# Kernel tuning notes

Hardware: AMD Instinct MI355X
Metric: run time of the kernel (lower is better)

The kernel has to match this reference:

```python
import jax, jax.numpy as jnp
import numpy as np

B, C, L = 8192, 256, 80          # nodes(batch), channels = out_channels*4, seq_len
OUT, HID, FD = 64, 128, 128      # out_channels, hidden dims, feature_dim
WIN, STR = 10, 5                 # sliding window
NW = (L - WIN) // STR + 1        # 15 windows
NT = B * NW                      # temporal nodes = 122880
E_S, E_T = 262144, 983040


def _param_shapes(prefix):
    return [(prefix + "l1_W", (C, HID)), (prefix + "l1_b", (HID,)), (prefix + "l1_Wr", (C, HID)),
            (prefix + "l2_W", (HID, OUT)), (prefix + "l2_b", (OUT,)), (prefix + "l2_Wr", (HID, OUT)),
            (prefix + "p1_W", (OUT, FD)), (prefix + "p1_b", (FD,)), (prefix + "p2_W", (FD, FD)), (prefix + "p2_b", (FD,))]


def setup_inputs():
    key = jax.random.key(0)
    shapes = _param_shapes("s_") + _param_shapes("t_")
    ks = jax.random.split(key, len(shapes) + 3)
    inp = {"x": jax.random.normal(ks[0], (B, C, L), jnp.float32),
           "spatial_edge_index": jax.random.randint(ks[1], (2, E_S), 0, B),
           "temporal_edge_index": jax.random.randint(ks[2], (2, E_T), 0, NT)}
    for i, (name, sh) in enumerate(shapes):
        scale = 1.0 / np.sqrt(sh[0]) if len(sh) == 2 else 0.01
        inp[name] = scale * jax.random.normal(ks[3 + i], sh, jnp.float32)
    return inp


def _l2norm(x):
    return x / jnp.maximum(jnp.linalg.norm(x, axis=1, keepdims=True), 1e-12)


def _sage(x, src, dst, Wl, b, Wr, n):
    # PyG SAGEConv (mean aggr): lin_l(mean_{j->i} x_j) + lin_r(x_i)
    agg = jax.ops.segment_sum(x[src], dst, num_segments=n)
    cnt = jax.ops.segment_sum(jnp.ones((src.shape[0],), x.dtype), dst, num_segments=n)
    mean = agg / jnp.maximum(cnt, 1.0)[:, None]
    return mean @ Wl + b + x @ Wr


def _encoder(x, ei, p, n):
    src, dst = ei[0], ei[1]
    h = jax.nn.relu(_sage(x, src, dst, p[0], p[1], p[2], n))
    h = _sage(h, src, dst, p[3], p[4], p[5], n)
    return _l2norm(h)


def _proj(x, W1, b1, W2, b2):
    return _l2norm(jax.nn.relu(x @ W1 + b1) @ W2 + b2)


def _forward(x, sp, tp, spatial_edge_index, temporal_edge_index):
    feats = x  # feature_extractor = identity
    node_x = feats.mean(axis=-1)                     # [B, C]
    s_emb = _encoder(node_x, spatial_edge_index, sp[:6], B)
    s_proj = _proj(s_emb, *sp[6:])
    # sliding window mean reduction, vectorized
    starts = jnp.arange(0, L - WIN + 1, STR)
    idx = starts[:, None] + jnp.arange(WIN)
    red = feats[:, :, idx].mean(axis=-1)             # [B, C, NW]
    red = red.transpose(0, 2, 1).reshape(NT, C)      # [B*NW, C]
    t_emb = _encoder(red, temporal_edge_index, tp[:6], NT)
    t_emb = t_emb.reshape(B, NW, OUT).mean(axis=1)   # [B, OUT]
    t_proj = _proj(t_emb, *tp[6:])
    return s_proj, t_proj


def reference(x, spatial_edge_index, temporal_edge_index,
              s_l1_W, s_l1_b, s_l1_Wr, s_l2_W, s_l2_b, s_l2_Wr, s_p1_W, s_p1_b, s_p2_W, s_p2_b,
              t_l1_W, t_l1_b, t_l1_Wr, t_l2_W, t_l2_b, t_l2_Wr, t_p1_W, t_p1_b, t_p2_W, t_p2_b):
    sp = (s_l1_W, s_l1_b, s_l1_Wr, s_l2_W, s_l2_b, s_l2_Wr, s_p1_W, s_p1_b, s_p2_W, s_p2_b)
    tp = (t_l1_W, t_l1_b, t_l1_Wr, t_l2_W, t_l2_b, t_l2_Wr, t_p1_W, t_p1_b, t_p2_W, t_p2_b)
    return _forward(x, sp, tp, spatial_edge_index, temporal_edge_index)
```

## Files before the change

kernel.cpp:

```cpp
#include <hip/hip_runtime.h>

#define B_    8192
#define C_    256
#define L_    80
#define OUT_  64
#define HID_  128
#define FD_   128
#define NW_   15
#define NT_   122880
#define E_S_  262144
#define E_T_  983040

__global__ __launch_bounds__(256) void k_reduce_x(const float* __restrict__ x,
                                                  float* __restrict__ node_x,
                                                  float* __restrict__ red) {
    int gid = blockIdx.x * 256 + threadIdx.x;
    const float4* row4 = reinterpret_cast<const float4*>(x + (size_t)gid * L_);
    float v[L_];
#pragma unroll
    for (int i = 0; i < L_ / 4; ++i) {
        float4 t = row4[i];
        v[4*i+0] = t.x; v[4*i+1] = t.y; v[4*i+2] = t.z; v[4*i+3] = t.w;
    }
    float s5[16];
    float tot = 0.f;
#pragma unroll
    for (int j = 0; j < 16; ++j) {
        float s = 0.f;
#pragma unroll
        for (int k = 0; k < 5; ++k) s += v[5*j + k];
        s5[j] = s; tot += s;
    }
    node_x[gid] = tot * (1.f / L_);
    int b = gid >> 8;
    int c = gid & 255;
#pragma unroll
    for (int w = 0; w < NW_; ++w)
        red[((size_t)(b * NW_ + w)) * C_ + c] = (s5[w] + s5[w + 1]) * 0.1f;
}

#define BM 64
#define BN 64
#define BK 16
__global__ __launch_bounds__(256) void k_gemm(const float* __restrict__ A,
                                              const float* __restrict__ W,
                                              const float* __restrict__ bias,
                                              float* __restrict__ Co,
                                              int N, int K, int M, int relu) {
    __shared__ float As[BK][BM];
    __shared__ float Ws[BK][BN];
    int t = threadIdx.x;
    int row0 = blockIdx.x * BM;
    int col0 = blockIdx.y * BN;
    int lr = t >> 2;
    int lk = (t & 3) * 4;
    int wk = t >> 4;
    int wc = (t & 15) * 4;
    int ty = t >> 4;
    int tx = t & 15;
    float acc[4][4] = {};
    for (int k0 = 0; k0 < K; k0 += BK) {
        float4 av = *reinterpret_cast<const float4*>(&A[(size_t)(row0 + lr) * K + k0 + lk]);
        float4 wv = *reinterpret_cast<const float4*>(&W[(size_t)(k0 + wk) * M + col0 + wc]);
        __syncthreads();
        As[lk + 0][lr] = av.x; As[lk + 1][lr] = av.y;
        As[lk + 2][lr] = av.z; As[lk + 3][lr] = av.w;
        *reinterpret_cast<float4*>(&Ws[wk][wc]) = wv;
        __syncthreads();
#pragma unroll
        for (int kk = 0; kk < BK; ++kk) {
            float4 a  = *reinterpret_cast<const float4*>(&As[kk][ty * 4]);
            float4 w4 = *reinterpret_cast<const float4*>(&Ws[kk][tx * 4]);
            acc[0][0] += a.x * w4.x; acc[0][1] += a.x * w4.y; acc[0][2] += a.x * w4.z; acc[0][3] += a.x * w4.w;
            acc[1][0] += a.y * w4.x; acc[1][1] += a.y * w4.y; acc[1][2] += a.y * w4.z; acc[1][3] += a.y * w4.w;
            acc[2][0] += a.z * w4.x; acc[2][1] += a.z * w4.y; acc[2][2] += a.z * w4.z; acc[2][3] += a.z * w4.w;
            acc[3][0] += a.w * w4.x; acc[3][1] += a.w * w4.y; acc[3][2] += a.w * w4.z; acc[3][3] += a.w * w4.w;
        }
    }
    int cbase = col0 + tx * 4;
    float4 bv = make_float4(0.f, 0.f, 0.f, 0.f);
    if (bias) bv = *reinterpret_cast<const float4*>(&bias[cbase]);
#pragma unroll
    for (int i = 0; i < 4; ++i) {
        int r = row0 + ty * 4 + i;
        float4 o;
        o.x = acc[i][0] + bv.x; o.y = acc[i][1] + bv.y;
        o.z = acc[i][2] + bv.z; o.w = acc[i][3] + bv.w;
        if (relu) {
            o.x = fmaxf(o.x, 0.f); o.y = fmaxf(o.y, 0.f);
            o.z = fmaxf(o.z, 0.f); o.w = fmaxf(o.w, 0.f);
        }
        *reinterpret_cast<float4*>(&Co[(size_t)r * M + cbase]) = o;
    }
}

__global__ __launch_bounds__(256) void k_gemm_dual(const float* __restrict__ A,
                                                   const float* __restrict__ W1,
                                                   float* __restrict__ C1,
                                                   const float* __restrict__ W2,
                                                   const float* __restrict__ b2,
                                                   float* __restrict__ C2,
                                                   int N, int K, int M) {
    __shared__ float As[BK][BM];
    __shared__ float W1s[BK][BN];
    __shared__ float W2s[BK][BN];
    int t = threadIdx.x;
    int row0 = blockIdx.x * BM;
    int col0 = blockIdx.y * BN;
    int lr = t >> 2;
    int lk = (t & 3) * 4;
    int wk = t >> 4;
    int wc = (t & 15) * 4;
    int ty = t >> 4;
    int tx = t & 15;
    float acc1[4][4] = {};
    float acc2[4][4] = {};
    for (int k0 = 0; k0 < K; k0 += BK) {
        float4 av  = *reinterpret_cast<const float4*>(&A[(size_t)(row0 + lr) * K + k0 + lk]);
        float4 w1v = *reinterpret_cast<const float4*>(&W1[(size_t)(k0 + wk) * M + col0 + wc]);
        float4 w2v = *reinterpret_cast<const float4*>(&W2[(size_t)(k0 + wk) * M + col0 + wc]);
        __syncthreads();
        As[lk + 0][lr] = av.x; As[lk + 1][lr] = av.y;
        As[lk + 2][lr] = av.z; As[lk + 3][lr] = av.w;
        *reinterpret_cast<float4*>(&W1s[wk][wc]) = w1v;
        *reinterpret_cast<float4*>(&W2s[wk][wc]) = w2v;
        __syncthreads();
#pragma unroll
        for (int kk = 0; kk < BK; ++kk) {
            float4 a  = *reinterpret_cast<const float4*>(&As[kk][ty * 4]);
            float4 u  = *reinterpret_cast<const float4*>(&W1s[kk][tx * 4]);
            float4 w  = *reinterpret_cast<const float4*>(&W2s[kk][tx * 4]);
            acc1[0][0] += a.x * u.x; acc1[0][1] += a.x * u.y; acc1[0][2] += a.x * u.z; acc1[0][3] += a.x * u.w;
            acc1[1][0] += a.y * u.x; acc1[1][1] += a.y * u.y; acc1[1][2] += a.y * u.z; acc1[1][3] += a.y * u.w;
            acc1[2][0] += a.z * u.x; acc1[2][1] += a.z * u.y; acc1[2][2] += a.z * u.z; acc1[2][3] += a.z * u.w;
            acc1[3][0] += a.w * u.x; acc1[3][1] += a.w * u.y; acc1[3][2] += a.w * u.z; acc1[3][3] += a.w * u.w;
            acc2[0][0] += a.x * w.x; acc2[0][1] += a.x * w.y; acc2[0][2] += a.x * w.z; acc2[0][3] += a.x * w.w;
            acc2[1][0] += a.y * w.x; acc2[1][1] += a.y * w.y; acc2[1][2] += a.y * w.z; acc2[1][3] += a.y * w.w;
            acc2[2][0] += a.z * w.x; acc2[2][1] += a.z * w.y; acc2[2][2] += a.z * w.z; acc2[2][3] += a.z * w.w;
            acc2[3][0] += a.w * w.x; acc2[3][1] += a.w * w.y; acc2[3][2] += a.w * w.z; acc2[3][3] += a.w * w.w;
        }
    }
    int cbase = col0 + tx * 4;
    float4 bv = *reinterpret_cast<const float4*>(&b2[cbase]);
#pragma unroll
    for (int i = 0; i < 4; ++i) {
        int r = row0 + ty * 4 + i;
        float4 o1, o2;
        o1.x = acc1[i][0]; o1.y = acc1[i][1]; o1.z = acc1[i][2]; o1.w = acc1[i][3];
        o2.x = acc2[i][0] + bv.x; o2.y = acc2[i][1] + bv.y;
        o2.z = acc2[i][2] + bv.z; o2.w = acc2[i][3] + bv.w;
        *reinterpret_cast<float4*>(&C1[(size_t)r * M + cbase]) = o1;
        *reinterpret_cast<float4*>(&C2[(size_t)r * M + cbase]) = o2;
    }
}

__global__ __launch_bounds__(256) void k_cnt(const int* __restrict__ dst,
                                             int* __restrict__ cnt, int E) {
    int g = blockIdx.x * 256 + threadIdx.x;
    if (g < E) atomicAdd(&cnt[dst[g]], 1);
}

__global__ __launch_bounds__(256) void k_scan_blk(const int* __restrict__ cnt,
                                                  int* __restrict__ rs,
                                                  int* __restrict__ bsum, int N) {
    __shared__ int s[256];
    int g = blockIdx.x * 256 + threadIdx.x;
    int v = (g < N) ? cnt[g] : 0;
    s[threadIdx.x] = v;
    __syncthreads();
    for (int off = 1; off < 256; off <<= 1) {
        int t = (threadIdx.x >= off) ? s[threadIdx.x - off] : 0;
        __syncthreads();
        s[threadIdx.x] += t;
        __syncthreads();
    }
    if (g < N) rs[g] = s[threadIdx.x] - v;
    if (threadIdx.x == 255) bsum[blockIdx.x] = s[255];
}

__global__ void k_scan_top(int* __restrict__ bsum, int nb) {
    if (threadIdx.x == 0 && blockIdx.x == 0) {
        int acc = 0;
        for (int i = 0; i < nb; ++i) { int v = bsum[i]; bsum[i] = acc; acc += v; }
    }
}

__global__ __launch_bounds__(256) void k_scan_add(int* __restrict__ rs,
                                                  const int* __restrict__ bsum,
                                                  int* __restrict__ fill, int N) {
    int g = blockIdx.x * 256 + threadIdx.x;
    if (g < N) {
        int v = rs[g] + bsum[blockIdx.x];
        rs[g] = v;
        fill[g] = v;
    }
}

__global__ __launch_bounds__(256) void k_scatter(const int* __restrict__ src,
                                                 const int* __restrict__ dst,
                                                 int* __restrict__ fill,
                                                 int* __restrict__ csr, int E) {
    int g = blockIdx.x * 256 + threadIdx.x;
    if (g < E) {
        int p = atomicAdd(&fill[dst[g]], 1);
        csr[p] = src[g];
    }
}

__global__ __launch_bounds__(256) void k_agg128(const int* __restrict__ rs,
                                                const int* __restrict__ cnt,
                                                const int* __restrict__ csr,
                                                const float* __restrict__ Y,
                                                const float* __restrict__ Z,
                                                float* __restrict__ Hout, int N) {
    int wid = (blockIdx.x * 256 + threadIdx.x) >> 6;
    int lane = threadIdx.x & 63;
    if (wid >= N) return;
    int s0 = rs[wid], c = cnt[wid];
    float2 acc = make_float2(0.f, 0.f);
    int j = 0;
    for (; j + 1 < c; j += 2) {
        int sa = csr[s0 + j], sb = csr[s0 + j + 1];
        float2 va = *reinterpret_cast<const float2*>(&Y[(size_t)sa * 128 + lane * 2]);
        float2 vb = *reinterpret_cast<const float2*>(&Y[(size_t)sb * 128 + lane * 2]);
        acc.x += va.x + vb.x; acc.y += va.y + vb.y;
    }
    if (j < c) {
        int sa = csr[s0 + j];
        float2 va = *reinterpret_cast<const float2*>(&Y[(size_t)sa * 128 + lane * 2]);
        acc.x += va.x; acc.y += va.y;
    }
    float rc = 1.f / fmaxf((float)c, 1.f);
    size_t idx = (size_t)wid * 128 + lane * 2;
    float2 z = *reinterpret_cast<const float2*>(&Z[idx]);
    float2 o;
    o.x = fmaxf(acc.x * rc + z.x, 0.f);
    o.y = fmaxf(acc.y * rc + z.y, 0.f);
    *reinterpret_cast<float2*>(&Hout[idx]) = o;
}

__global__ __launch_bounds__(256) void k_agg64n(const int* __restrict__ rs,
                                                const int* __restrict__ cnt,
                                                const int* __restrict__ csr,
                                                const float* __restrict__ Y,
                                                const float* __restrict__ Z,
                                                float* __restrict__ emb, int N) {
    int wid = (blockIdx.x * 256 + threadIdx.x) >> 6;
    int lane = threadIdx.x & 63;
    if (wid >= N) return;
    int s0 = rs[wid], c = cnt[wid];
    float acc = 0.f;
    int j = 0;
    for (; j + 1 < c; j += 2) {
        int sa = csr[s0 + j], sb = csr[s0 + j + 1];
        acc += Y[(size_t)sa * 64 + lane] + Y[(size_t)sb * 64 + lane];
    }
    if (j < c) acc += Y[(size_t)csr[s0 + j] * 64 + lane];
    float rc = 1.f / fmaxf((float)c, 1.f);
    size_t idx = (size_t)wid * 64 + lane;
    float v = acc * rc + Z[idx];
    float ss = v * v;
#pragma unroll
    for (int m = 32; m; m >>= 1) ss += __shfl_xor(ss, m, 64);
    float inv = 1.f / fmaxf(sqrtf(ss), 1e-12f);
    emb[idx] = v * inv;
}

__global__ __launch_bounds__(256) void k_l2n128(const float* __restrict__ in,
                                                float* __restrict__ out, int N) {
    int wid = (blockIdx.x * 256 + threadIdx.x) >> 6;
    int lane = threadIdx.x & 63;
    if (wid >= N) return;
    size_t idx = (size_t)wid * 128 + lane * 2;
    float2 v = *reinterpret_cast<const float2*>(&in[idx]);
    float ss = v.x * v.x + v.y * v.y;
#pragma unroll
    for (int m = 32; m; m >>= 1) ss += __shfl_xor(ss, m, 64);
    float inv = 1.f / fmaxf(sqrtf(ss), 1e-12f);
    float2 o; o.x = v.x * inv; o.y = v.y * inv;
    *reinterpret_cast<float2*>(&out[idx]) = o;
}

__global__ __launch_bounds__(256) void k_tmean(const float* __restrict__ emb,
                                               float* __restrict__ out) {
    int gid = blockIdx.x * 256 + threadIdx.x;
    if (gid >= B_ * OUT_) return;
    int b = gid >> 6;
    int o = gid & 63;
    float s = 0.f;
#pragma unroll
    for (int w = 0; w < NW_; ++w) s += emb[((size_t)(b * NW_ + w)) * OUT_ + o];
    out[gid] = s * (1.f / NW_);
}

extern "C" void kernel_launch(void* const* d_in, const int* in_sizes, int n_in,
                              void* d_out, int out_size, void* d_ws, size_t ws_size,
                              hipStream_t stream) {
    const float* x      = (const float*)d_in[0];
    const int*   s_ei   = (const int*)d_in[1];
    const int*   t_ei   = (const int*)d_in[2];
    const float* s_l1_W  = (const float*)d_in[3];
    const float* s_l1_b  = (const float*)d_in[4];
    const float* s_l1_Wr = (const float*)d_in[5];
    const float* s_l2_W  = (const float*)d_in[6];
    const float* s_l2_b  = (const float*)d_in[7];
    const float* s_l2_Wr = (const float*)d_in[8];
    const float* s_p1_W  = (const float*)d_in[9];
    const float* s_p1_b  = (const float*)d_in[10];
    const float* s_p2_W  = (const float*)d_in[11];
    const float* s_p2_b  = (const float*)d_in[12];
    const float* t_l1_W  = (const float*)d_in[13];
    const float* t_l1_b  = (const float*)d_in[14];
    const float* t_l1_Wr = (const float*)d_in[15];
    const float* t_l2_W  = (const float*)d_in[16];
    const float* t_l2_b  = (const float*)d_in[17];
    const float* t_l2_Wr = (const float*)d_in[18];
    const float* t_p1_W  = (const float*)d_in[19];
    const float* t_p1_b  = (const float*)d_in[20];
    const float* t_p2_W  = (const float*)d_in[21];
    const float* t_p2_b  = (const float*)d_in[22];

    const int* s_src = s_ei, *s_dst = s_ei + E_S_;
    const int* t_src = t_ei, *t_dst = t_ei + E_T_;

    float* ws   = (float*)d_ws;
    float* dout = (float*)d_out;

    float* red    = ws + 0;
    float* nodex  = ws + 31457280;
    float* sY     = ws + 33554432;
    float* sZ     = ws + 34603008;
    float* sH     = ws + 35651584;
    float* s2Y    = ws + 36700160;
    float* s2Z    = ws + 37224448;
    float* sE     = ws + 37748736;
    float* sP     = ws + 38273024;
    float* sT     = ws + 39321600;
    float* tY     = ws + 31457280;
    float* tZ     = ws + 47185920;
    float* tH     = ws + 0;
    float* t2Y    = ws + 15728640;
    float* t2Z    = ws + 23592960;
    float* tE     = ws + 31457280;
    float* tM     = ws + 39321600;
    float* tP     = ws + 39845888;
    float* tT     = ws + 40894464;
    int* s_cnt  = (int*)(ws + 62914560);
    int* s_rs   = (int*)(ws + 62922752);
    int* s_fill = (int*)(ws + 62930944);
    int* s_csr  = (int*)(ws + 62939136);
    int* t_cnt  = (int*)(ws + 63201280);
    int* t_rs   = (int*)(ws + 63324160);
    int* t_fill = (int*)(ws + 63447040);
    int* t_csr  = (int*)(ws + 63569920);
    int* bsum   = (int*)(ws + 64552960);

    k_reduce_x<<<(B_ * C_) / 256, 256, 0, stream>>>(x, nodex, red);

    hipMemsetAsync(s_cnt, 0, (size_t)B_ * 4, stream);
    k_cnt<<<E_S_ / 256, 256, 0, stream>>>(s_dst, s_cnt, E_S_);
    k_scan_blk<<<B_ / 256, 256, 0, stream>>>(s_cnt, s_rs, bsum, B_);
    k_scan_top<<<1, 1, 0, stream>>>(bsum, B_ / 256);
    k_scan_add<<<B_ / 256, 256, 0, stream>>>(s_rs, bsum, s_fill, B_);
    k_scatter<<<E_S_ / 256, 256, 0, stream>>>(s_src, s_dst, s_fill, s_csr, E_S_);

    k_gemm_dual<<<dim3(B_ / 64, HID_ / 64), 256, 0, stream>>>(nodex, s_l1_W, sY, s_l1_Wr, s_l1_b, sZ, B_, C_, HID_);
    k_agg128<<<B_ / 4, 256, 0, stream>>>(s_rs, s_cnt, s_csr, sY, sZ, sH, B_);
    k_gemm_dual<<<dim3(B_ / 64, OUT_ / 64), 256, 0, stream>>>(sH, s_l2_W, s2Y, s_l2_Wr, s_l2_b, s2Z, B_, HID_, OUT_);
    k_agg64n<<<B_ / 4, 256, 0, stream>>>(s_rs, s_cnt, s_csr, s2Y, s2Z, sE, B_);
    k_gemm<<<dim3(B_ / 64, FD_ / 64), 256, 0, stream>>>(sE, s_p1_W, s_p1_b, sP, B_, OUT_, FD_, 1);
    k_gemm<<<dim3(B_ / 64, FD_ / 64), 256, 0, stream>>>(sP, s_p2_W, s_p2_b, sT, B_, FD_, FD_, 0);
    k_l2n128<<<B_ / 4, 256, 0, stream>>>(sT, dout, B_);

    hipMemsetAsync(t_cnt, 0, (size_t)NT_ * 4, stream);
    k_cnt<<<E_T_ / 256, 256, 0, stream>>>(t_dst, t_cnt, E_T_);
    k_scan_blk<<<NT_ / 256, 256, 0, stream>>>(t_cnt, t_rs, bsum, NT_);
    k_scan_top<<<1, 1, 0, stream>>>(bsum, NT_ / 256);
    k_scan_add<<<NT_ / 256, 256, 0, stream>>>(t_rs, bsum, t_fill, NT_);
    k_scatter<<<E_T_ / 256, 256, 0, stream>>>(t_src, t_dst, t_fill, t_csr, E_T_);

    k_gemm_dual<<<dim3(NT_ / 64, HID_ / 64), 256, 0, stream>>>(red, t_l1_W, tY, t_l1_Wr, t_l1_b, tZ, NT_, C_, HID_);
    k_agg128<<<NT_ / 4, 256, 0, stream>>>(t_rs, t_cnt, t_csr, tY, tZ, tH, NT_);
    k_gemm_dual<<<dim3(NT_ / 64, OUT_ / 64), 256, 0, stream>>>(tH, t_l2_W, t2Y, t_l2_Wr, t_l2_b, t2Z, NT_, HID_, OUT_);
    k_agg64n<<<NT_ / 4, 256, 0, stream>>>(t_rs, t_cnt, t_csr, t2Y, t2Z, tE, NT_);
    k_tmean<<<(B_ * OUT_) / 256, 256, 0, stream>>>(tE, tM);
    k_gemm<<<dim3(B_ / 64, FD_ / 64), 256, 0, stream>>>(tM, t_p1_W, t_p1_b, tP, B_, OUT_, FD_, 1);
    k_gemm<<<dim3(B_ / 64, FD_ / 64), 256, 0, stream>>>(tP, t_p2_W, t_p2_b, tT, B_, FD_, FD_, 0);
    k_l2n128<<<B_ / 4, 256, 0, stream>>>(tT, dout + (size_t)B_ * FD_, B_);
}
```

Measured before the change: 1.704 ms.

## Run SAGE linear layers on MFMA with split-bf16 hi/lo emulation of fp32

Replaces the fp32 SIMT dual GEMMs of both SAGE layers with bf16 MFMA kernels that use a hi/lo split (three MFMAs per tile) to approximate fp32 accuracy. Activations are written as bf16 hi/lo pairs by the reduction and aggregation kernels, and the weights are converted and transposed once per call by a new kernel. The single-thread top-level scan becomes a parallel 512-thread scan. The aim is to move the large temporal GEMMs onto matrix cores, at the cost of twice the activation traffic for the hi/lo planes, separate launches per weight matrix, and a small accuracy loss from dropping the lo*lo term.

```diff
diff --git a/kernel.cpp b/kernel.cpp
--- a/kernel.cpp
+++ b/kernel.cpp
@@ -11,9 +11,24 @@
 #define E_S_  262144
 #define E_T_  983040
 
+typedef unsigned short ushort_t;
+typedef __attribute__((ext_vector_type(8))) short bf16x8;
+typedef __attribute__((ext_vector_type(4))) float f32x4;
+
+__device__ inline void split_bf16(float a, ushort_t& h, ushort_t& l) {
+    unsigned u = __float_as_uint(a);
+    unsigned hb = (u + 0x7FFFu + ((u >> 16) & 1u)) & 0xFFFF0000u;
+    h = (ushort_t)(hb >> 16);
+    float r = a - __uint_as_float(hb);
+    unsigned v = __float_as_uint(r);
+    l = (ushort_t)((v + 0x7FFFu + ((v >> 16) & 1u)) >> 16);
+}
+
 __global__ __launch_bounds__(256) void k_reduce_x(const float* __restrict__ x,
-                                                  float* __restrict__ node_x,
-                                                  float* __restrict__ red) {
+                                                  ushort_t* __restrict__ node_h,
+                                                  ushort_t* __restrict__ node_l,
+                                                  ushort_t* __restrict__ red_h,
+                                                  ushort_t* __restrict__ red_l) {
     int gid = blockIdx.x * 256 + threadIdx.x;
     const float4* row4 = reinterpret_cast<const float4*>(x + (size_t)gid * L_);
     float v[L_];
@@ -31,12 +46,256 @@
         for (int k = 0; k < 5; ++k) s += v[5*j + k];
         s5[j] = s; tot += s;
     }
-    node_x[gid] = tot * (1.f / L_);
+    ushort_t h, l;
+    split_bf16(tot * (1.f / L_), h, l);
+    node_h[gid] = h; node_l[gid] = l;
     int b = gid >> 8;
     int c = gid & 255;
 #pragma unroll
-    for (int w = 0; w < NW_; ++w)
-        red[((size_t)(b * NW_ + w)) * C_ + c] = (s5[w] + s5[w + 1]) * 0.1f;
+    for (int w = 0; w < NW_; ++w) {
+        split_bf16((s5[w] + s5[w + 1]) * 0.1f, h, l);
+        size_t idx = ((size_t)(b * NW_ + w)) * C_ + c;
+        red_h[idx] = h; red_l[idx] = l;
+    }
+}
+
+__global__ __launch_bounds__(256) void k_conv_all(
+        const float* __restrict__ w0, const float* __restrict__ w1,
+        const float* __restrict__ w2, const float* __restrict__ w3,
+        const float* __restrict__ w4, const float* __restrict__ w5,
+        const float* __restrict__ w6, const float* __restrict__ w7,
+        ushort_t* __restrict__ blob) {
+    const int bstart[9] = {0, 128, 256, 288, 320, 448, 576, 608, 640};
+    const int Ks[8]     = {256, 256, 128, 128, 256, 256, 128, 128};
+    const int hoff[8]   = {0, 65536, 131072, 147456, 163840, 229376, 294912, 311296};
+    int blk = blockIdx.x;
+    int seg = 0;
+    while (blk >= bstart[seg + 1]) ++seg;
+    const float* W = (seg == 0) ? w0 : (seg == 1) ? w1 : (seg == 2) ? w2 : (seg == 3) ? w3
+                   : (seg == 4) ? w4 : (seg == 5) ? w5 : (seg == 6) ? w6 : w7;
+    int K = Ks[seg];
+    int nel = (bstart[seg + 1] - bstart[seg]) * 256;
+    int M = nel / K;
+    int g = (blk - bstart[seg]) * 256 + threadIdx.x;
+    int k = g / M, m = g - k * M;
+    ushort_t h, l;
+    split_bf16(W[g], h, l);
+    blob[hoff[seg] + m * K + k] = h;
+    blob[hoff[seg] + nel + m * K + k] = l;
+}
+
+template<int KTOT, int NF>
+__global__ __launch_bounds__(256, 2) void k_mfma_gemm(const ushort_t* __restrict__ Ah,
+                                                      const ushort_t* __restrict__ Al,
+                                                      const ushort_t* __restrict__ Wh,
+                                                      const ushort_t* __restrict__ Wl,
+                                                      const float* __restrict__ bias,
+                                                      float* __restrict__ C) {
+    constexpr int BN = NF * 32;
+    __shared__ short sAh[128][72], sAl[128][72], sWh[128][72], sWl[128][72];
+    int t = threadIdx.x;
+    int row0 = blockIdx.x * 128;
+    int wid = t >> 6, lane = t & 63;
+    int wr = wid >> 1, wc = wid & 1;
+    int lrow = lane & 15, lkg = lane >> 4;
+
+    f32x4 acc[4][NF];
+#pragma unroll
+    for (int mi = 0; mi < 4; ++mi)
+#pragma unroll
+        for (int ni = 0; ni < NF; ++ni) {
+            acc[mi][ni].x = 0.f; acc[mi][ni].y = 0.f;
+            acc[mi][ni].z = 0.f; acc[mi][ni].w = 0.f;
+        }
+
+    for (int k0 = 0; k0 < KTOT; k0 += 64) {
+        __syncthreads();
+#pragma unroll
+        for (int i = 0; i < 4; ++i) {
+            int ch = t + i * 256;
+            int r = ch >> 3, c = ch & 7;
+            *reinterpret_cast<int4*>(&sAh[r][c * 8]) =
+                *reinterpret_cast<const int4*>(&Ah[(size_t)(row0 + r) * KTOT + k0 + c * 8]);
+            *reinterpret_cast<int4*>(&sAl[r][c * 8]) =
+                *reinterpret_cast<const int4*>(&Al[(size_t)(row0 + r) * KTOT + k0 + c * 8]);
+        }
+#pragma unroll
+        for (int i = 0; i < 4; ++i) {
+            int ch = t + i * 256;
+            int r = ch >> 3, c = ch & 7;
+            if (r < BN) {
+                *reinterpret_cast<int4*>(&sWh[r][c * 8]) =
+                    *reinterpret_cast<const int4*>(&Wh[(size_t)r * KTOT + k0 + c * 8]);
+                *reinterpret_cast<int4*>(&sWl[r][c * 8]) =
+                    *reinterpret_cast<const int4*>(&Wl[(size_t)r * KTOT + k0 + c * 8]);
+            }
+        }
+        __syncthreads();
+#pragma unroll
+        for (int ks = 0; ks < 64; ks += 32) {
+            bf16x8 ah[4], al[4], wh[NF], wl[NF];
+            int kk = ks + lkg * 8;
+#pragma unroll
+            for (int mi = 0; mi < 4; ++mi) {
+                int r = wr * 64 + mi * 16 + lrow;
+                ah[mi] = *reinterpret_cast<const bf16x8*>(&sAh[r][kk]);
+                al[mi] = *reinterpret_cast<const bf16x8*>(&sAl[r][kk]);
+            }
+#pragma unroll
+            for (int ni = 0; ni < NF; ++ni) {
+                int r = wc * (NF * 16) + ni * 16 + lrow;
+                wh[ni] = *reinterpret_cast<const bf16x8*>(&sWh[r][kk]);
+                wl[ni] = *reinterpret_cast<const bf16x8*>(&sWl[r][kk]);
+            }
+#pragma unroll
+            for (int mi = 0; mi < 4; ++mi)
+#pragma unroll
+                for (int ni = 0; ni < NF; ++ni) {
+                    acc[mi][ni] = __builtin_amdgcn_mfma_f32_16x16x32_bf16(ah[mi], wh[ni], acc[mi][ni], 0, 0, 0);
+                    acc[mi][ni] = __builtin_amdgcn_mfma_f32_16x16x32_bf16(ah[mi], wl[ni], acc[mi][ni], 0, 0, 0);
+                    acc[mi][ni] = __builtin_amdgcn_mfma_f32_16x16x32_bf16(al[mi], wh[ni], acc[mi][ni], 0, 0, 0);
+                }
+        }
+    }
+    float bv[NF];
+#pragma unroll
+    for (int ni = 0; ni < NF; ++ni) {
+        int gcol = wc * (NF * 16) + ni * 16 + lrow;
+        bv[ni] = bias ? bias[gcol] : 0.f;
+    }
+#pragma unroll
+    for (int mi = 0; mi < 4; ++mi)
+#pragma unroll
+        for (int ni = 0; ni < NF; ++ni) {
+            int gcol = wc * (NF * 16) + ni * 16 + lrow;
+#pragma unroll
+            for (int j = 0; j < 4; ++j) {
+                int grow = row0 + wr * 64 + mi * 16 + lkg * 4 + j;
+                C[(size_t)grow * BN + gcol] = acc[mi][ni][j] + bv[ni];
+            }
+        }
+}
+
+__global__ __launch_bounds__(256) void k_cnt(const int* __restrict__ dst,
+                                             int* __restrict__ cnt, int E) {
+    int g = blockIdx.x * 256 + threadIdx.x;
+    if (g < E) atomicAdd(&cnt[dst[g]], 1);
+}
+
+__global__ __launch_bounds__(256) void k_scan_blk(const int* __restrict__ cnt,
+                                                  int* __restrict__ rs,
+                                                  int* __restrict__ bsum, int N) {
+    __shared__ int s[256];
+    int g = blockIdx.x * 256 + threadIdx.x;
+    int v = (g < N) ? cnt[g] : 0;
+    s[threadIdx.x] = v;
+    __syncthreads();
+    for (int off = 1; off < 256; off <<= 1) {
+        int t = (threadIdx.x >= off) ? s[threadIdx.x - off] : 0;
+        __syncthreads();
+        s[threadIdx.x] += t;
+        __syncthreads();
+    }
+    if (g < N) rs[g] = s[threadIdx.x] - v;
+    if (threadIdx.x == 255) bsum[blockIdx.x] = s[255];
+}
+
+__global__ __launch_bounds__(512) void k_scan_top(int* __restrict__ bsum, int nb) {
+    __shared__ int s[512];
+    int t = threadIdx.x;
+    int v = (t < nb) ? bsum[t] : 0;
+    s[t] = v;
+    __syncthreads();
+    for (int off = 1; off < 512; off <<= 1) {
+        int x = (t >= off) ? s[t - off] : 0;
+        __syncthreads();
+        s[t] += x;
+        __syncthreads();
+    }
+    if (t < nb) bsum[t] = s[t] - v;
+}
+
+__global__ __launch_bounds__(256) void k_scan_add(int* __restrict__ rs,
+                                                  const int* __restrict__ bsum,
+                                                  int* __restrict__ fill, int N) {
+    int g = blockIdx.x * 256 + threadIdx.x;
+    if (g < N) {
+        int v = rs[g] + bsum[blockIdx.x];
+        rs[g] = v;
+        fill[g] = v;
+    }
+}
+
+__global__ __launch_bounds__(256) void k_scatter(const int* __restrict__ src,
+                                                 const int* __restrict__ dst,
+                                                 int* __restrict__ fill,
+                                                 int* __restrict__ csr, int E) {
+    int g = blockIdx.x * 256 + threadIdx.x;
+    if (g < E) {
+        int p = atomicAdd(&fill[dst[g]], 1);
+        csr[p] = src[g];
+    }
+}
+
+__global__ __launch_bounds__(256) void k_agg128(const int* __restrict__ rs,
+                                                const int* __restrict__ cnt,
+                                                const int* __restrict__ csr,
+                                                const float* __restrict__ Y,
+                                                const float* __restrict__ Z,
+                                                ushort_t* __restrict__ Hh,
+                                                ushort_t* __restrict__ Hl, int N) {
+    int wid = (blockIdx.x * 256 + threadIdx.x) >> 6;
+    int lane = threadIdx.x & 63;
+    if (wid >= N) return;
+    int s0 = rs[wid], c = cnt[wid];
+    float2 acc = make_float2(0.f, 0.f);
+    int j = 0;
+    for (; j + 1 < c; j += 2) {
+        int sa = csr[s0 + j], sb = csr[s0 + j + 1];
+        float2 va = *reinterpret_cast<const float2*>(&Y[(size_t)sa * 128 + lane * 2]);
+        float2 vb = *reinterpret_cast<const float2*>(&Y[(size_t)sb * 128 + lane * 2]);
+        acc.x += va.x + vb.x; acc.y += va.y + vb.y;
+    }
+    if (j < c) {
+        int sa = csr[s0 + j];
+        float2 va = *reinterpret_cast<const float2*>(&Y[(size_t)sa * 128 + lane * 2]);
+        acc.x += va.x; acc.y += va.y;
+    }
+    float rc = 1.f / fmaxf((float)c, 1.f);
+    size_t idx = (size_t)wid * 128 + lane * 2;
+    float2 z = *reinterpret_cast<const float2*>(&Z[idx]);
+    float ox = fmaxf(acc.x * rc + z.x, 0.f);
+    float oy = fmaxf(acc.y * rc + z.y, 0.f);
+    ushort_t h, l;
+    split_bf16(ox, h, l); Hh[idx] = h;     Hl[idx] = l;
+    split_bf16(oy, h, l); Hh[idx + 1] = h; Hl[idx + 1] = l;
+}
+
+__global__ __launch_bounds__(256) void k_agg64n(const int* __restrict__ rs,
+                                                const int* __restrict__ cnt,
+                                                const int* __restrict__ csr,
+                                                const float* __restrict__ Y,
+                                                const float* __restrict__ Z,
+                                                float* __restrict__ emb, int N) {
+    int wid = (blockIdx.x * 256 + threadIdx.x) >> 6;
+    int lane = threadIdx.x & 63;
+    if (wid >= N) return;
+    int s0 = rs[wid], c = cnt[wid];
+    float acc = 0.f;
+    int j = 0;
+    for (; j + 1 < c; j += 2) {
+        int sa = csr[s0 + j], sb = csr[s0 + j + 1];
+        acc += Y[(size_t)sa * 64 + lane] + Y[(size_t)sb * 64 + lane];
+    }
+    if (j < c) acc += Y[(size_t)csr[s0 + j] * 64 + lane];
+    float rc = 1.f / fmaxf((float)c, 1.f);
+    size_t idx = (size_t)wid * 64 + lane;
+    float v = acc * rc + Z[idx];
+    float ss = v * v;
+#pragma unroll
+    for (int m = 32; m; m >>= 1) ss += __shfl_xor(ss, m, 64);
+    float inv = 1.f / fmaxf(sqrtf(ss), 1e-12f);
+    emb[idx] = v * inv;
 }
 
 #define BM 64
@@ -92,178 +351,6 @@
         }
         *reinterpret_cast<float4*>(&Co[(size_t)r * M + cbase]) = o;
     }
-}
-
-__global__ __launch_bounds__(256) void k_gemm_dual(const float* __restrict__ A,
-                                                   const float* __restrict__ W1,
-                                                   float* __restrict__ C1,
-                                                   const float* __restrict__ W2,
-                                                   const float* __restrict__ b2,
-                                                   float* __restrict__ C2,
-                                                   int N, int K, int M) {
-    __shared__ float As[BK][BM];
-    __shared__ float W1s[BK][BN];
-    __shared__ float W2s[BK][BN];
-    int t = threadIdx.x;
-    int row0 = blockIdx.x * BM;
-    int col0 = blockIdx.y * BN;
-    int lr = t >> 2;
-    int lk = (t & 3) * 4;
-    int wk = t >> 4;
-    int wc = (t & 15) * 4;
-    int ty = t >> 4;
-    int tx = t & 15;
-    float acc1[4][4] = {};
-    float acc2[4][4] = {};
-    for (int k0 = 0; k0 < K; k0 += BK) {
-        float4 av  = *reinterpret_cast<const float4*>(&A[(size_t)(row0 + lr) * K + k0 + lk]);
-        float4 w1v = *reinterpret_cast<const float4*>(&W1[(size_t)(k0 + wk) * M + col0 + wc]);
-        float4 w2v = *reinterpret_cast<const float4*>(&W2[(size_t)(k0 + wk) * M + col0 + wc]);
-        __syncthreads();
-        As[lk + 0][lr] = av.x; As[lk + 1][lr] = av.y;
-        As[lk + 2][lr] = av.z; As[lk + 3][lr] = av.w;
-        *reinterpret_cast<float4*>(&W1s[wk][wc]) = w1v;
-        *reinterpret_cast<float4*>(&W2s[wk][wc]) = w2v;
-        __syncthreads();
-#pragma unroll
-        for (int kk = 0; kk < BK; ++kk) {
-            float4 a  = *reinterpret_cast<const float4*>(&As[kk][ty * 4]);
-            float4 u  = *reinterpret_cast<const float4*>(&W1s[kk][tx * 4]);
-            float4 w  = *reinterpret_cast<const float4*>(&W2s[kk][tx * 4]);
-            acc1[0][0] += a.x * u.x; acc1[0][1] += a.x * u.y; acc1[0][2] += a.x * u.z; acc1[0][3] += a.x * u.w;
-            acc1[1][0] += a.y * u.x; acc1[1][1] += a.y * u.y; acc1[1][2] += a.y * u.z; acc1[1][3] += a.y * u.w;
-            acc1[2][0] += a.z * u.x; acc1[2][1] += a.z * u.y; acc1[2][2] += a.z * u.z; acc1[2][3] += a.z * u.w;
-            acc1[3][0] += a.w * u.x; acc1[3][1] += a.w * u.y; acc1[3][2] += a.w * u.z; acc1[3][3] += a.w * u.w;
-            acc2[0][0] += a.x * w.x; acc2[0][1] += a.x * w.y; acc2[0][2] += a.x * w.z; acc2[0][3] += a.x * w.w;
-            acc2[1][0] += a.y * w.x; acc2[1][1] += a.y * w.y; acc2[1][2] += a.y * w.z; acc2[1][3] += a.y * w.w;
-            acc2[2][0] += a.z * w.x; acc2[2][1] += a.z * w.y; acc2[2][2] += a.z * w.z; acc2[2][3] += a.z * w.w;
-            acc2[3][0] += a.w * w.x; acc2[3][1] += a.w * w.y; acc2[3][2] += a.w * w.z; acc2[3][3] += a.w * w.w;
-        }
-    }
-    int cbase = col0 + tx * 4;
-    float4 bv = *reinterpret_cast<const float4*>(&b2[cbase]);
-#pragma unroll
-    for (int i = 0; i < 4; ++i) {
-        int r = row0 + ty * 4 + i;
-        float4 o1, o2;
-        o1.x = acc1[i][0]; o1.y = acc1[i][1]; o1.z = acc1[i][2]; o1.w = acc1[i][3];
-        o2.x = acc2[i][0] + bv.x; o2.y = acc2[i][1] + bv.y;
-        o2.z = acc2[i][2] + bv.z; o2.w = acc2[i][3] + bv.w;
-        *reinterpret_cast<float4*>(&C1[(size_t)r * M + cbase]) = o1;
-        *reinterpret_cast<float4*>(&C2[(size_t)r * M + cbase]) = o2;
-    }
-}
-
-__global__ __launch_bounds__(256) void k_cnt(const int* __restrict__ dst,
-                                             int* __restrict__ cnt, int E) {
-    int g = blockIdx.x * 256 + threadIdx.x;
-    if (g < E) atomicAdd(&cnt[dst[g]], 1);
-}
-
-__global__ __launch_bounds__(256) void k_scan_blk(const int* __restrict__ cnt,
-                                                  int* __restrict__ rs,
-                                                  int* __restrict__ bsum, int N) {
-    __shared__ int s[256];
-    int g = blockIdx.x * 256 + threadIdx.x;
-    int v = (g < N) ? cnt[g] : 0;
-    s[threadIdx.x] = v;
-    __syncthreads();
-    for (int off = 1; off < 256; off <<= 1) {
-        int t = (threadIdx.x >= off) ? s[threadIdx.x - off] : 0;
-        __syncthreads();
-        s[threadIdx.x] += t;
-        __syncthreads();
-    }
-    if (g < N) rs[g] = s[threadIdx.x] - v;
-    if (threadIdx.x == 255) bsum[blockIdx.x] = s[255];
-}
-
-__global__ void k_scan_top(int* __restrict__ bsum, int nb) {
-    if (threadIdx.x == 0 && blockIdx.x == 0) {
-        int acc = 0;
-        for (int i = 0; i < nb; ++i) { int v = bsum[i]; bsum[i] = acc; acc += v; }
-    }
-}
-
-__global__ __launch_bounds__(256) void k_scan_add(int* __restrict__ rs,
-                                                  const int* __restrict__ bsum,
-                                                  int* __restrict__ fill, int N) {
-    int g = blockIdx.x * 256 + threadIdx.x;
-    if (g < N) {
-        int v = rs[g] + bsum[blockIdx.x];
-        rs[g] = v;
-        fill[g] = v;
-    }
-}
-
-__global__ __launch_bounds__(256) void k_scatter(const int* __restrict__ src,
-                                                 const int* __restrict__ dst,
-                                                 int* __restrict__ fill,
-                                                 int* __restrict__ csr, int E) {
-    int g = blockIdx.x * 256 + threadIdx.x;
-    if (g < E) {
-        int p = atomicAdd(&fill[dst[g]], 1);
-        csr[p] = src[g];
-    }
-}
-
-__global__ __launch_bounds__(256) void k_agg128(const int* __restrict__ rs,
-                                                const int* __restrict__ cnt,
-                                                const int* __restrict__ csr,
-                                                const float* __restrict__ Y,
-                                                const float* __restrict__ Z,
-                                                float* __restrict__ Hout, int N) {
-    int wid = (blockIdx.x * 256 + threadIdx.x) >> 6;
-    int lane = threadIdx.x & 63;
-    if (wid >= N) return;
-    int s0 = rs[wid], c = cnt[wid];
-    float2 acc = make_float2(0.f, 0.f);
-    int j = 0;
-    for (; j + 1 < c; j += 2) {
-        int sa = csr[s0 + j], sb = csr[s0 + j + 1];
-        float2 va = *reinterpret_cast<const float2*>(&Y[(size_t)sa * 128 + lane * 2]);
-        float2 vb = *reinterpret_cast<const float2*>(&Y[(size_t)sb * 128 + lane * 2]);
-        acc.x += va.x + vb.x; acc.y += va.y + vb.y;
-    }
-    if (j < c) {
-        int sa = csr[s0 + j];
-        float2 va = *reinterpret_cast<const float2*>(&Y[(size_t)sa * 128 + lane * 2]);
-        acc.x += va.x; acc.y += va.y;
-    }
-    float rc = 1.f / fmaxf((float)c, 1.f);
-    size_t idx = (size_t)wid * 128 + lane * 2;
-    float2 z = *reinterpret_cast<const float2*>(&Z[idx]);
-    float2 o;
-    o.x = fmaxf(acc.x * rc + z.x, 0.f);
-    o.y = fmaxf(acc.y * rc + z.y, 0.f);
-    *reinterpret_cast<float2*>(&Hout[idx]) = o;
-}
-
-__global__ __launch_bounds__(256) void k_agg64n(const int* __restrict__ rs,
-                                                const int* __restrict__ cnt,
-                                                const int* __restrict__ csr,
-                                                const float* __restrict__ Y,
-                                                const float* __restrict__ Z,
-                                                float* __restrict__ emb, int N) {
-    int wid = (blockIdx.x * 256 + threadIdx.x) >> 6;
-    int lane = threadIdx.x & 63;
-    if (wid >= N) return;
-    int s0 = rs[wid], c = cnt[wid];
-    float acc = 0.f;
-    int j = 0;
-    for (; j + 1 < c; j += 2) {
-        int sa = csr[s0 + j], sb = csr[s0 + j + 1];
-        acc += Y[(size_t)sa * 64 + lane] + Y[(size_t)sb * 64 + lane];
-    }
-    if (j < c) acc += Y[(size_t)csr[s0 + j] * 64 + lane];
-    float rc = 1.f / fmaxf((float)c, 1.f);
-    size_t idx = (size_t)wid * 64 + lane;
-    float v = acc * rc + Z[idx];
-    float ss = v * v;
-#pragma unroll
-    for (int m = 32; m; m >>= 1) ss += __shfl_xor(ss, m, 64);
-    float inv = 1.f / fmaxf(sqrtf(ss), 1e-12f);
-    emb[idx] = v * inv;
 }
 
 __global__ __launch_bounds__(256) void k_l2n128(const float* __restrict__ in,
@@ -326,47 +413,66 @@
     float* ws   = (float*)d_ws;
     float* dout = (float*)d_out;
 
-    float* red    = ws + 0;
-    float* nodex  = ws + 31457280;
-    float* sY     = ws + 33554432;
-    float* sZ     = ws + 34603008;
-    float* sH     = ws + 35651584;
-    float* s2Y    = ws + 36700160;
-    float* s2Z    = ws + 37224448;
-    float* sE     = ws + 37748736;
-    float* sP     = ws + 38273024;
-    float* sT     = ws + 39321600;
-    float* tY     = ws + 31457280;
-    float* tZ     = ws + 47185920;
-    float* tH     = ws + 0;
-    float* t2Y    = ws + 15728640;
-    float* t2Z    = ws + 23592960;
-    float* tE     = ws + 31457280;
-    float* tM     = ws + 39321600;
-    float* tP     = ws + 39845888;
-    float* tT     = ws + 40894464;
-    int* s_cnt  = (int*)(ws + 62914560);
-    int* s_rs   = (int*)(ws + 62922752);
-    int* s_fill = (int*)(ws + 62930944);
-    int* s_csr  = (int*)(ws + 62939136);
-    int* t_cnt  = (int*)(ws + 63201280);
-    int* t_rs   = (int*)(ws + 63324160);
-    int* t_fill = (int*)(ws + 63447040);
-    int* t_csr  = (int*)(ws + 63569920);
-    int* bsum   = (int*)(ws + 64552960);
-
-    k_reduce_x<<<(B_ * C_) / 256, 256, 0, stream>>>(x, nodex, red);
+    size_t o = 0;
+    auto alloc = [&](size_t n) { float* r = ws + o; o += n; return r; };
+    ushort_t* red_h  = (ushort_t*)alloc(15728640);
+    ushort_t* red_l  = (ushort_t*)alloc(15728640);
+    ushort_t* node_h = (ushort_t*)alloc(1048576);
+    ushort_t* node_l = (ushort_t*)alloc(1048576);
+    float* sY  = alloc(1048576);
+    float* sZ  = alloc(1048576);
+    ushort_t* sHh = (ushort_t*)alloc(524288);
+    ushort_t* sHl = (ushort_t*)alloc(524288);
+    float* s2Y = alloc(524288);
+    float* s2Z = alloc(524288);
+    float* sE  = alloc(524288);
+    float* sP  = alloc(1048576);
+    float* sT  = alloc(1048576);
+    float* tY  = alloc(15728640);
+    float* tZ  = alloc(15728640);
+    ushort_t* tHh = (ushort_t*)alloc(7864320);
+    ushort_t* tHl = (ushort_t*)alloc(7864320);
+    float* t2Y = alloc(7864320);
+    float* t2Z = alloc(7864320);
+    float* tE  = alloc(7864320);
+    float* tM  = alloc(524288);
+    float* tP  = alloc(1048576);
+    float* tT  = alloc(1048576);
+    ushort_t* wblob = (ushort_t*)alloc(163840);
+    ushort_t* swl1h = wblob + 0;      ushort_t* swl1l = wblob + 32768;
+    ushort_t* swr1h = wblob + 65536;  ushort_t* swr1l = wblob + 98304;
+    ushort_t* swl2h = wblob + 131072; ushort_t* swl2l = wblob + 139264;
+    ushort_t* swr2h = wblob + 147456; ushort_t* swr2l = wblob + 155648;
+    ushort_t* twl1h = wblob + 163840; ushort_t* twl1l = wblob + 196608;
+    ushort_t* twr1h = wblob + 229376; ushort_t* twr1l = wblob + 262144;
+    ushort_t* twl2h = wblob + 294912; ushort_t* twl2l = wblob + 303104;
+    ushort_t* twr2h = wblob + 311296; ushort_t* twr2l = wblob + 319488;
+    int* s_cnt  = (int*)alloc(8192);
+    int* s_rs   = (int*)alloc(8192);
+    int* s_fill = (int*)alloc(8192);
+    int* s_csr  = (int*)alloc(262144);
+    int* t_cnt  = (int*)alloc(122880);
+    int* t_rs   = (int*)alloc(122880);
+    int* t_fill = (int*)alloc(122880);
+    int* t_csr  = (int*)alloc(983040);
+    int* bsum   = (int*)alloc(512);
+
+    k_reduce_x<<<(B_ * C_) / 256, 256, 0, stream>>>(x, node_h, node_l, red_h, red_l);
+    k_conv_all<<<640, 256, 0, stream>>>(s_l1_W, s_l1_Wr, s_l2_W, s_l2_Wr,
+                                        t_l1_W, t_l1_Wr, t_l2_W, t_l2_Wr, wblob);
 
     hipMemsetAsync(s_cnt, 0, (size_t)B_ * 4, stream);
     k_cnt<<<E_S_ / 256, 256, 0, stream>>>(s_dst, s_cnt, E_S_);
     k_scan_blk<<<B_ / 256, 256, 0, stream>>>(s_cnt, s_rs, bsum, B_);
-    k_scan_top<<<1, 1, 0, stream>>>(bsum, B_ / 256);
+    k_scan_top<<<1, 512, 0, stream>>>(bsum, B_ / 256);
     k_scan_add<<<B_ / 256, 256, 0, stream>>>(s_rs, bsum, s_fill, B_);
     k_scatter<<<E_S_ / 256, 256, 0, stream>>>(s_src, s_dst, s_fill, s_csr, E_S_);
 
-    k_gemm_dual<<<dim3(B_ / 64, HID_ / 64), 256, 0, stream>>>(nodex, s_l1_W, sY, s_l1_Wr, s_l1_b, sZ, B_, C_, HID_);
-    k_agg128<<<B_ / 4, 256, 0, stream>>>(s_rs, s_cnt, s_csr, sY, sZ, sH, B_);
-    k_gemm_dual<<<dim3(B_ / 64, OUT_ / 64), 256, 0, stream>>>(sH, s_l2_W, s2Y, s_l2_Wr, s_l2_b, s2Z, B_, HID_, OUT_);
+    k_mfma_gemm<256, 4><<<B_ / 128, 256, 0, stream>>>(node_h, node_l, swl1h, swl1l, nullptr, sY);
+    k_mfma_gemm<256, 4><<<B_ / 128, 256, 0, stream>>>(node_h, node_l, swr1h, swr1l, s_l1_b, sZ);
+    k_agg128<<<B_ / 4, 256, 0, stream>>>(s_rs, s_cnt, s_csr, sY, sZ, sHh, sHl, B_);
+    k_mfma_gemm<128, 2><<<B_ / 128, 256, 0, stream>>>(sHh, sHl, swl2h, swl2l, nullptr, s2Y);
+    k_mfma_gemm<128, 2><<<B_ / 128, 256, 0, stream>>>(sHh, sHl, swr2h, swr2l, s_l2_b, s2Z);
     k_agg64n<<<B_ / 4, 256, 0, stream>>>(s_rs, s_cnt, s_csr, s2Y, s2Z, sE, B_);
     k_gemm<<<dim3(B_ / 64, FD_ / 64), 256, 0, stream>>>(sE, s_p1_W, s_p1_b, sP, B_, OUT_, FD_, 1);
     k_gemm<<<dim3(B_ / 64, FD_ / 64), 256, 0, stream>>>(sP, s_p2_W, s_p2_b, sT, B_, FD_, FD_, 0);
@@ -375,13 +481,15 @@
     hipMemsetAsync(t_cnt, 0, (size_t)NT_ * 4, stream);
     k_cnt<<<E_T_ / 256, 256, 0, stream>>>(t_dst, t_cnt, E_T_);
     k_scan_blk<<<NT_ / 256, 256, 0, stream>>>(t_cnt, t_rs, bsum, NT_);
-    k_scan_top<<<1, 1, 0, stream>>>(bsum, NT_ / 256);
+    k_scan_top<<<1, 512, 0, stream>>>(bsum, NT_ / 256);
     k_scan_add<<<NT_ / 256, 256, 0, stream>>>(t_rs, bsum, t_fill, NT_);
     k_scatter<<<E_T_ / 256, 256, 0, stream>>>(t_src, t_dst, t_fill, t_csr, E_T_);
 
-    k_gemm_dual<<<dim3(NT_ / 64, HID_ / 64), 256, 0, stream>>>(red, t_l1_W, tY, t_l1_Wr, t_l1_b, tZ, NT_, C_, HID_);
-    k_agg128<<<NT_ / 4, 256, 0, stream>>>(t_rs, t_cnt, t_csr, tY, tZ, tH, NT_);
-    k_gemm_dual<<<dim3(NT_ / 64, OUT_ / 64), 256, 0, stream>>>(tH, t_l2_W, t2Y, t_l2_Wr, t_l2_b, t2Z, NT_, HID_, OUT_);
+    k_mfma_gemm<256, 4><<<NT_ / 128, 256, 0, stream>>>(red_h, red_l, twl1h, twl1l, nullptr, tY);
+    k_mfma_gemm<256, 4><<<NT_ / 128, 256, 0, stream>>>(red_h, red_l, twr1h, twr1l, t_l1_b, tZ);
+    k_agg128<<<NT_ / 4, 256, 0, stream>>>(t_rs, t_cnt, t_csr, tY, tZ, tHh, tHl, NT_);
+    k_mfma_gemm<128, 2><<<NT_ / 128, 256, 0, stream>>>(tHh, tHl, twl2h, twl2l, nullptr, t2Y);
+    k_mfma_gemm<128, 2><<<NT_ / 128, 256, 0, stream>>>(tHh, tHl, twr2h, twr2l, t_l2_b, t2Z);
     k_agg64n<<<NT_ / 4, 256, 0, stream>>>(t_rs, t_cnt, t_csr, t2Y, t2Z, tE, NT_);
     k_tmean<<<(B_ * OUT_) / 256, 256, 0, stream>>>(tE, tM);
     k_gemm<<<dim3(B_ / 64, FD_ / 64), 256, 0, stream>>>(tM, t_p1_W, t_p1_b, tP, B_, OUT_, FD_, 1);
```

After: 1.519 ms. 10.8% less time.
